# Performance work log

Hardware: AMD Instinct MI355X
Metric: run time of the kernel (lower is better)

## Reference

```python
import jax, jax.numpy as jnp
import numpy as np

C = 32           # in_channels
KH, KW = 3, 3    # kernel_range
SHIFT = 1
NP = KH * KW


def conv2d(x, w, b, pad):
    # x: NCHW, w: OIHW
    y = jax.lax.conv_general_dilated(
        x, w, window_strides=(1, 1), padding=[(pad, pad), (pad, pad)],
        dimension_numbers=('NCHW', 'OIHW', 'NCHW'))
    return y + b[None, :, None, None]


def setup_inputs() -> dict:
    key = jax.random.key(0)
    ks = jax.random.split(key, 14)
    p = lambda k, shape: (jax.random.normal(k, shape, dtype=jnp.float32) * 0.02)
    inp = {
        'x':  jax.random.normal(ks[0], (4, C, 256, 256), dtype=jnp.float32),
        'wk': p(ks[1], (C * NP, C, 1, 1)), 'bk': p(ks[2], (C * NP,)),
        'wv': p(ks[3], (C * NP, C, 1, 1)), 'bv': p(ks[4], (C * NP,)),
        'wq': p(ks[5], (C, C, 1, 1)),      'bq': p(ks[6], (C,)),
        'w1': p(ks[7], (C, C, 3, 3)),      'b1': p(ks[8], (C,)),
        'w2': p(ks[9], (2 * C, C, 3, 3)),  'b2': p(ks[10], (2 * C,)),
        'w3': p(ks[11], (C, 2 * C, 3, 3)), 'b3': p(ks[12], (C,)),
    }
    return inp


def reference(x, wk, bk, wv, bv, wq, bq, w1, b1, w2, b2, w3, b3):
    B, D, H, W = x.shape
    h_half, w_half = KH // 2, KW // 2
    ph, pw = h_half * SHIFT, w_half * SHIFT

    x_k = conv2d(x, wk, bk, 0)  # (B, D*NP, H, W)
    x_v = conv2d(x, wv, bv, 0)
    x_q = conv2d(x, wq, bq, 0)  # (B, D, H, W)

    pad4 = ((0, 0), (0, 0), (ph, ph), (pw, pw))
    x_k = jnp.pad(x_k, pad4)
    x_v = jnp.pad(x_v, pad4)
    mask_pad = jnp.pad(jnp.ones((B, 1, H, W), x.dtype), pad4)

    k_ls, v_ls, m_ls = [], [], []
    layer = 0
    for i in range(-h_half, h_half + 1):
        for j in range(-w_half, w_half + 1):
            r0 = ph + i * SHIFT
            c0 = pw + j * SHIFT
            k_ls.append(x_k[:, layer * D:(layer + 1) * D, r0:r0 + H, c0:c0 + W])
            v_ls.append(x_v[:, layer * D:(layer + 1) * D, r0:r0 + H, c0:c0 + W])
            m_ls.append(mask_pad[:, :, r0:r0 + H, c0:c0 + W])
            layer += 1

    # Faithful to torch .view semantics: flat row-major reshape, NOT a permute.
    k = jnp.stack(k_ls, axis=1).reshape(B * H * W, NP, D)   # (B,NP,D,H,W) -> flat
    v = jnp.stack(v_ls, axis=1).reshape(B * H * W, NP, D)
    m = jnp.stack(m_ls, axis=1).reshape(B * H * W, NP, 1)
    q = x_q.reshape(B * H * W, 1, D)                         # (B,D,H,W) -> flat

    scores = jnp.matmul(k, jnp.swapaxes(q, -1, -2)) * m / 8.0  # (N, NP, 1)
    alpha = jax.nn.softmax(scores, axis=1)
    res = jnp.matmul(jnp.swapaxes(alpha, -1, -2), v)           # (N, 1, D)
    t = res.reshape(B, D, H, W)

    t = jax.nn.relu(conv2d(t, w1, b1, 1))
    t = jax.nn.relu(conv2d(t, w2, b2, 1))
    t = jax.nn.relu(conv2d(t, w3, b3, 1))
    return t
```

## Files before the change

### kernel.cpp

```cpp
#include <hip/hip_runtime.h>
#include <hip/hip_bf16.h>

#define B_ 4
#define C_ 32
#define H_ 256
#define W_ 256
#define S_ 65536
#define NP_ 9
#define OC_ 288
#define PR 258
#define PWN 264
#define XGUARD 260
#define XSTRIDE 66056

using bf16 = __hip_bfloat16;
typedef __attribute__((ext_vector_type(8)))  short  short8;
typedef __attribute__((ext_vector_type(4)))  short  short4_t;
typedef __attribute__((ext_vector_type(2)))  short  short2_t;
typedef __attribute__((ext_vector_type(16))) float  f32x16;

__device__ __forceinline__ float b2f(short s) {
    return __uint_as_float(((unsigned)(unsigned short)s) << 16);
}

template<int IC, int OC>
__device__ __forceinline__ void prepA_body(int fid, const float* __restrict__ w,
                                           bf16* __restrict__ apk)
{
    constexpr int NK = 9 * IC / 16;
    int tile = fid >> 9;
    int l = (fid >> 3) & 63;
    int j = fid & 7;
    int mt = tile / NK;
    int ks = tile - mt * NK;
    int q = l >> 5;
    int oc = mt * 32 + (l & 31);
    int k = ks * 16 + q * 8 + j;
    int tap = k / IC;
    int ic = k - tap * IC;
    apk[fid] = __float2bfloat16(w[((oc * IC + ic) * 3 + tap / 3) * 3 + tap % 3]);
}

template<int G>
__device__ __forceinline__ void zerob_body(int b, int p, uint4* __restrict__ buf)
{
    int gran;
    if (p < 2 * PWN * G) {
        int row = (p < PWN * G) ? 0 : 257;
        int rem = p % (PWN * G);
        gran = row * PWN * G + rem;
    } else {
        int p2 = p - 2 * PWN * G;
        int col = (p2 < 256 * G) ? 0 : 257;
        int rem = p2 % (256 * G);
        int r = rem / G + 1;
        int icg = rem - (rem / G) * G;
        gran = (r * PWN + col) * G + icg;
    }
    buf[(size_t)b * PR * PWN * G + gran] = uint4{0, 0, 0, 0};
}

__global__ __launch_bounds__(256) void k_prep(
    const float* __restrict__ wk, const float* __restrict__ wv,
    const float* __restrict__ wq,
    const float* __restrict__ w1, const float* __restrict__ w2,
    const float* __restrict__ w3,
    bf16* __restrict__ apk0, bf16* __restrict__ apk1,
    bf16* __restrict__ apk2, bf16* __restrict__ apk3,
    uint4* __restrict__ tA, uint4* __restrict__ t1, uint4* __restrict__ t2,
    uint4* __restrict__ xb16)
{
    int idx = blockIdx.x * 256 + threadIdx.x;
    if (idx < 19456) {
        int j    = idx & 7;
        int lane = (idx >> 3) & 63;
        int ks   = (idx >> 9) & 1;
        int mt   = idx >> 10;
        int oc = lane & 31;
        int ic = ks * 16 + (lane >> 5) * 8 + j;
        const float* w; int ocg;
        if (mt < 9)       { w = wk; ocg = mt * 32 + oc; }
        else if (mt < 18) { w = wv; ocg = (mt - 9) * 32 + oc; }
        else              { w = wq; ocg = oc; }
        apk0[idx] = __float2bfloat16(w[ocg * C_ + ic]);
    } else if (idx < 28672) {
        prepA_body<32, 32>(idx - 19456, w1, apk1);
    } else if (idx < 47104) {
        prepA_body<32, 64>(idx - 28672, w2, apk2);
    } else if (idx < 65536) {
        prepA_body<64, 32>(idx - 47104, w3, apk3);
    } else if (idx < 82176) {
        int i5 = idx - 65536;
        zerob_body<4>(i5 / 4160, i5 % 4160, tA);
    } else if (idx < 98816) {
        int i6 = idx - 82176;
        zerob_body<4>(i6 / 4160, i6 % 4160, t1);
    } else if (idx < 132096) {
        int i7 = idx - 98816;
        zerob_body<8>(i7 / 8320, i7 % 8320, t2);
    } else if (idx < 142464) {
        int i8 = idx - 132096;
        size_t off;
        if (i8 < 8320) {
            int b = i8 / 2080, r = i8 - b * 2080;
            if (r < 1040) off = (size_t)b * (XSTRIDE * 4) + r;
            else          off = ((size_t)b * XSTRIDE + XGUARD + 65536) * 4 + (r - 1040);
        } else {
            off = (size_t)(4 * XSTRIDE) * 4 + (i8 - 8320);
        }
        xb16[off] = uint4{0, 0, 0, 0};
    }
}

__global__ __launch_bounds__(256) void k_q(
    const float* __restrict__ x, const bf16* __restrict__ apk,
    const float* __restrict__ bq, bf16* __restrict__ xqs, bf16* __restrict__ xb16)
{
    __shared__ bf16 lbuf[32][140];
    int bh  = blockIdx.x >> 9;
    int blk = blockIdx.x & 511;
    int pixw0 = blk << 7;
    int tid  = threadIdx.x;
    int wvi  = tid >> 6;
    int lane = tid & 63;
    int col  = lane & 31, q = lane >> 5;
    int pix  = pixw0 + wvi * 32 + col;

    const float* xb = x + (size_t)bh * (C_ * S_);

    short8 bfrag[2];
#pragma unroll
    for (int kk = 0; kk < 2; ++kk)
#pragma unroll
        for (int j = 0; j < 8; ++j) {
            bf16 h = __float2bfloat16(xb[(size_t)(kk * 16 + q * 8 + j) * S_ + pix]);
            bfrag[kk][j] = *reinterpret_cast<short*>(&h);
        }

    {
        bf16* xr = xb16 + ((size_t)bh * XSTRIDE + XGUARD + pix) * 32;
        *reinterpret_cast<short8*>(xr + (q << 3))       = bfrag[0];
        *reinterpret_cast<short8*>(xr + ((2 + q) << 3)) = bfrag[1];
    }

    const short8* apkv = reinterpret_cast<const short8*>(apk);
    f32x16 acc = {};
    acc = __builtin_amdgcn_mfma_f32_32x32x16_bf16(bfrag[0], apkv[(18 * 2 + 0) * 64 + lane], acc, 0, 0, 0);
    acc = __builtin_amdgcn_mfma_f32_32x32x16_bf16(bfrag[1], apkv[(18 * 2 + 1) * 64 + lane], acc, 0, 0, 0);
    float bbv = bq[col];
#pragma unroll
    for (int g4 = 0; g4 < 4; ++g4) {
        short4_t sv;
#pragma unroll
        for (int j = 0; j < 4; ++j) {
            bf16 hb = __float2bfloat16(acc[g4 * 4 + j] + bbv);
            sv[j] = *reinterpret_cast<short*>(&hb);
        }
        *reinterpret_cast<short4_t*>(&lbuf[col][wvi * 32 + 8 * g4 + 4 * q]) = sv;
    }
    __syncthreads();
    int ch0 = tid >> 4, chk = tid & 15, ch1 = ch0 + 16;
    short8 v0 = *reinterpret_cast<const short8*>(&lbuf[ch0][chk * 8]);
    short8 v1 = *reinterpret_cast<const short8*>(&lbuf[ch1][chk * 8]);
    int tb = (pixw0 >> 5) + (chk >> 2);
    int G2 = chk & 3;
    bf16* qb = xqs + (size_t)bh * (32 * S_);
    short4_t lo0 = {v0[0], v0[1], v0[2], v0[3]}, hi0 = {v0[4], v0[5], v0[6], v0[7]};
    short4_t lo1 = {v1[0], v1[1], v1[2], v1[3]}, hi1 = {v1[4], v1[5], v1[6], v1[7]};
    *reinterpret_cast<short4_t*>(qb + (ch0 * 2048 + tb) * 32 + G2 * 4)      = lo0;
    *reinterpret_cast<short4_t*>(qb + (ch0 * 2048 + tb) * 32 + 16 + G2 * 4) = hi0;
    *reinterpret_cast<short4_t*>(qb + (ch1 * 2048 + tb) * 32 + G2 * 4)      = lo1;
    *reinterpret_cast<short4_t*>(qb + (ch1 * 2048 + tb) * 32 + 16 + G2 * 4) = hi1;
}


#define DO_TILE(T, SQ)                                                                \
{                                                                                     \
    int Tg = tgbase + (T);                                                            \
    if (Tg < 2048) {                                                                  \
        unsigned n = (unsigned)plane_base + ((unsigned)Tg << 5);                      \
        unsigned tl = n / 288u;                                                       \
        const bf16* qp = xqb + ((size_t)tl << 5) + (q << 4);                          \
        short8 qA = *reinterpret_cast<const short8*>(qp);                             \
        short8 qB = *reinterpret_cast<const short8*>(qp + 8);                         \
        int xib = ((T) << 5) + 257 + shf + col;                                       \
        int swx = (xib ^ (xib >> 2)) & 3;                                             \
        short8 fa = *reinterpret_cast<const short8*>(&xs[xib * 4 + (q ^ swx)]);       \
        short8 fb = *reinterpret_cast<const short8*>(&xs[xib * 4 + ((2 + q) ^ swx)]); \
        bool hbad  = ((((T) << 5) < hb_lo) || (((T) << 5) >= hb_hi));                 \
        bool tb_lo = (dj == -1) && ((Tg & 7) == 0);                                   \
        bool tb_hi = (dj == 1) && ((Tg & 7) == 7);                                    \
        if (tb_lo && q == 0) qA[0] = 0;                                               \
        if (tb_hi && q == 1) qB[7] = 0;                                               \
        f32x16 ka = {bK, bK, bK, bK, bK, bK, bK, bK, bK, bK, bK, bK, bK, bK, bK, bK}; \
        ka = __builtin_amdgcn_mfma_f32_32x32x16_bf16(fa, apkv[(p * 2 + 0) * 64 + lane], ka, 0, 0, 0); \
        ka = __builtin_amdgcn_mfma_f32_32x32x16_bf16(fb, apkv[(p * 2 + 1) * 64 + lane], ka, 0, 0, 0); \
        float dot = 0.f;                                                              \
        _Pragma("unroll")                                                             \
        for (int j3 = 0; j3 < 4; ++j3) {                                              \
            dot += ka[j3]      * b2f(qA[j3]);                                         \
            dot += ka[4 + j3]  * b2f(qA[4 + j3]);                                     \
            dot += ka[8 + j3]  * b2f(qB[j3]);                                         \
            dot += ka[12 + j3] * b2f(qB[4 + j3]);                                     \
        }                                                                             \
        dot += __shfl_xor(dot, 32);                                                   \
        if (q == (SQ)) scL[(T) * 32 + col] = dot;                                     \
        f32x16 vh = {bV, bV, bV, bV, bV, bV, bV, bV, bV, bV, bV, bV, bV, bV, bV, bV}; \
        vh = __builtin_amdgcn_mfma_f32_32x32x16_bf16(fa, apkv[((9 + p) * 2 + 0) * 64 + lane], vh, 0, 0, 0); \
        vh = __builtin_amdgcn_mfma_f32_32x32x16_bf16(fb, apkv[((9 + p) * 2 + 1) * 64 + lane], vh, 0, 0, 0); \
        _Pragma("unroll")                                                             \
        for (int G2 = 0; G2 < 4; ++G2) {                                              \
            short4_t sv;                                                              \
            _Pragma("unroll")                                                         \
            for (int j3 = 0; j3 < 4; ++j3) {                                          \
                float val = hbad ? 0.f : vh[G2 * 4 + j3];                             \
                bf16 hcv = __float2bfloat16(val);                                     \
                sv[j3] = *reinterpret_cast<short*>(&hcv);                             \
            }                                                                         \
            if (G2 == 0 && tb_lo && q == 0) sv[0] = 0;                                \
            if (G2 == 3 && tb_hi && q == 1) sv[3] = 0;                                \
            *reinterpret_cast<short4_t*>(kvB + col * 1616 +                           \
                ((((T) << 2) + (G2 ^ xcol)) << 4) + q * 8) = sv;                      \
        }                                                                             \
    }                                                                                 \
}

__global__ __launch_bounds__(1024, 4) void k_fused(
    const bf16* __restrict__ xb16,
    const bf16* __restrict__ apk,
    const float* __restrict__ bk, const float* __restrict__ bv,
    const bf16* __restrict__ xqs,
    bf16* __restrict__ att)
{
    extern __shared__ char smem_raw[];
    uint4* xs  = reinterpret_cast<uint4*>(smem_raw);
    char*  kvB = smem_raw + 84096;
    float* scL = reinterpret_cast<float*>(smem_raw + 135808);
    unsigned short* scM = reinterpret_cast<unsigned short*>(smem_raw + 139008);

    int bb = blockIdx.x >> 7;
    int s0 = (blockIdx.x & 127) << 9;
    int tgbase = s0 >> 5;

    int tid  = threadIdx.x;
    int lane = tid & 63;
    int wv   = tid >> 6;
    int col  = lane & 31;
    int q    = lane >> 5;
    int xcol = (col >> 3) & 3;

    size_t qbase = ((size_t)bb << 21);
    const bf16* xqb = xqs + qbase;
    const short8* apkv = reinterpret_cast<const short8*>(apk);

    {
        const uint4* src = reinterpret_cast<const uint4*>(xb16) +
                           ((size_t)bb * XSTRIDE + XGUARD + s0 - 257) * 4;
        for (int i = tid; i < 5256; i += 1024) {
            int xi = i >> 2, g = i & 3;
            int sw = (xi ^ (xi >> 2)) & 3;
            xs[xi * 4 + (g ^ sw)] = src[i];
        }
    }

    if (tid < 576) {
        int krow = tid >= 288;
        int i2 = tid - (krow ? 288 : 0);
        int pp = i2 >> 5, dpc = i2 & 31;
        int plane_base_r = ((pp << 5) + dpc) << 16;
        unsigned tl = ((unsigned)(plane_base_r + s0 + 287)) / 288u + (unsigned)krow;
        int sk0 = (int)(tl * 288u) - plane_base_r;
        unsigned m = 0;
        if (sk0 < s0 + 512 && sk0 <= 65248) {
            m = 0x8000u;
#pragma unroll
            for (int seg = 0; seg < 9; ++seg) {
                int rm = (int)tl * 9 + seg;
                int pm = rm >> 16, sm = rm & 65535;
                int dim = pm / 3 - 1, djm = pm - (pm / 3) * 3 - 1;
                int hm = sm >> 8, wm = sm & 255;
                bool mval = ((unsigned)(hm + dim) < 256u) && ((unsigned)(wm + djm) < 256u);
                m |= (mval ? 1u : 0u) << seg;
            }
        }
        scM[tid] = (unsigned short)m;
    }
    __syncthreads();

    int sub   = tid & 15;
    int strip = tid >> 4;
    int dp    = strip & 31;
    int krow  = strip >> 5;
    int swz   = (dp >> 3) & 3;
    int vboff = dp * 1616 + (((sub >> 2) ^ swz) << 4) + ((sub >> 1) & 1) * 8 + (sub & 1) * 4;

#pragma unroll 1
    for (int p = 0; p < 9; ++p) {
        int di = p / 3 - 1, dj = p - (p / 3) * 3 - 1;
        int shf = di * 256 + dj;
        int hb_lo = (di == -1) ? (256 - s0) : (-0x40000000);
        int hb_hi = (di == 1) ? (65280 - s0) : 0x40000000;
        float bK = bk[p * 32 + col];
        float bV = bv[p * 32 + col];
        int plane_base = ((p << 5) + col) << 16;

        DO_TILE(wv, 0)
        if (wv < 9) { DO_TILE(wv + 16, 1) }
        __syncthreads();

        {
            unsigned mflags = scM[krow * 288 + p * 32 + dp];
            if (mflags & 0x8000u) {
                int plane_base_r = ((p << 5) + dp) << 16;
                unsigned tl = ((unsigned)(plane_base_r + s0 + 287)) / 288u + (unsigned)krow;
                int sk0 = (int)(tl * 288u) - plane_base_r;
                int t0 = (sk0 - s0) >> 5;
                float sc[9];
#pragma unroll
                for (int seg = 0; seg < 9; ++seg)
                    sc[seg] = ((mflags >> seg) & 1u) ? scL[(t0 + seg) * 32 + dp] * 0.125f : 0.f;
                float mx = sc[0];
#pragma unroll
                for (int s2 = 1; s2 < 9; ++s2) mx = fmaxf(mx, sc[s2]);
                float wgt[9];
                float sum = 0.f;
#pragma unroll
                for (int s2 = 0; s2 < 9; ++s2) { wgt[s2] = __expf(sc[s2] - mx); sum += wgt[s2]; }
                float inv_ = 1.f / sum;

                const char* vb = kvB + vboff + t0 * 64;
                float o0 = 0.f, o1 = 0.f;
#pragma unroll
                for (int seg = 0; seg < 9; ++seg) {
                    short2_t vg = *reinterpret_cast<const short2_t*>(vb + seg * 64);
                    float w_ = wgt[seg];
                    o0 += w_ * b2f(vg[0]);
                    o1 += w_ * b2f(vg[1]);
                }
                bf16 h0 = __float2bfloat16(o0 * inv_);
                bf16 h1 = __float2bfloat16(o1 * inv_);
                short2_t s2v = {*reinterpret_cast<short*>(&h0), *reinterpret_cast<short*>(&h1)};
                *reinterpret_cast<short2_t*>(att + qbase + ((size_t)tl << 5) + sub * 2) = s2v;
            }
        }
        __syncthreads();
    }
}

__global__ __launch_bounds__(320) void k_strad(
    const bf16* __restrict__ xb16,
    const float* __restrict__ wk, const float* __restrict__ bk,
    const float* __restrict__ wv, const float* __restrict__ bv,
    const bf16* __restrict__ xqs, bf16* __restrict__ att)
{
    __shared__ float kL[288], vL[288], qL[32], wgtL[10];
    int e = blockIdx.x;
    int b = e >> 8, i = e & 255;
    int g = i >> 3, u = i & 7;
    int tl = g * 2048 + (((2040 + u) * 1593) & 2047);
    int tid = threadIdx.x;

    if (tid < 288) {
        int f  = tl * 288 + tid;
        int cp = f >> 16;
        int sp = f & 65535;
        int tap = cp >> 5;
        int di = tap / 3 - 1, dj = tap - (tap / 3) * 3 - 1;
        int h = sp >> 8, w = sp & 255;
        bool valid = ((unsigned)(h + di) < 256u) && ((unsigned)(w + dj) < 256u);
        float kv_ = 0.f, vv_ = 0.f;
        if (valid) {
            int sx = sp + di * 256 + dj;
            const bf16* xp = xb16 + ((size_t)b * XSTRIDE + XGUARD + sx) * 32;
            const float* wkp = wk + cp * 32;
            const float* wvp = wv + cp * 32;
            float ks = bk[cp], vs = bv[cp];
            short8 xg[4];
#pragma unroll
            for (int gg = 0; gg < 4; ++gg)
                xg[gg] = *reinterpret_cast<const short8*>(xp + gg * 8);
#pragma unroll
            for (int gg = 0; gg < 4; ++gg)
#pragma unroll
                for (int j = 0; j < 8; ++j) {
                    float xv_ = b2f(xg[gg][j]);
                    ks += wkp[gg * 8 + j] * xv_;
                    vs += wvp[gg * 8 + j] * xv_;
                }
            kv_ = ks; vv_ = vs;
        }
        kL[tid] = kv_; vL[tid] = vv_;
    }
    if (tid < 32) {
        int pos = ((tid >> 2) & 1) * 16 + (tid >> 3) * 4 + (tid & 3);
        bf16 hv = xqs[(size_t)b * (32 * S_) + (size_t)tl * 32 + pos];
        qL[tid] = b2f(*reinterpret_cast<short*>(&hv));
    }
    __syncthreads();
    if (tid < 9) {
        float dot = 0.f;
#pragma unroll
        for (int d = 0; d < 32; ++d) dot += kL[tid * 32 + d] * qL[d];
        int rm = tl * 9 + tid;
        int pm = rm >> 16, sm = rm & 65535;
        int dim = pm / 3 - 1, djm = pm - (pm / 3) * 3 - 1;
        int hm = sm >> 8, wm = sm & 255;
        bool mval = ((unsigned)(hm + dim) < 256u) && ((unsigned)(wm + djm) < 256u);
        wgtL[tid] = mval ? dot * 0.125f : 0.f;
    }
    __syncthreads();
    if (tid == 0) {
        float mx = wgtL[0];
#pragma unroll
        for (int s2 = 1; s2 < 9; ++s2) mx = fmaxf(mx, wgtL[s2]);
        float sum = 0.f;
#pragma unroll
        for (int s2 = 0; s2 < 9; ++s2) { wgtL[s2] = __expf(wgtL[s2] - mx); sum += wgtL[s2]; }
        wgtL[9] = 1.f / sum;
    }
    __syncthreads();
    if (tid < 32) {
        float acc = 0.f;
#pragma unroll
        for (int seg = 0; seg < 9; ++seg) acc += wgtL[seg] * vL[seg * 32 + tid];
        att[(size_t)b * 2097152 + (size_t)tl * 32 + tid] = __float2bfloat16(acc * wgtL[9]);
    }
}

__global__ __launch_bounds__(256) void k_repack(
    const bf16* __restrict__ att, bf16* __restrict__ tA)
{
    int idx = blockIdx.x * 256 + threadIdx.x;
    int icg = idx & 3;
    int ps  = idx >> 2;
    int b = ps >> 16;
    int s = ps & 65535;
    const bf16* src = att + (size_t)b * (32 * S_) + icg * 8 * S_ + s;
    short8 v;
#pragma unroll
    for (int j = 0; j < 8; ++j)
        v[j] = *reinterpret_cast<const short*>(src + (size_t)j * S_);
    int row = (s >> 8) + 1, colp = (s & 255) + 1;
    *reinterpret_cast<short8*>(tA + ((size_t)((b * PR + row) * PWN + colp)) * 32 + icg * 8) = v;
}

template<int IC, int OC, bool NCHW_OUT>
__global__ __launch_bounds__(256) void k_conv3s(
    const bf16* __restrict__ in,
    const bf16* __restrict__ apk,
    const float* __restrict__ bs,
    void* __restrict__ outv)
{
    constexpr int G    = IC / 8;
    constexpr int M    = OC / 32;
    constexpr int KPT  = IC / 16;
    constexpr int NK   = 9 * KPT;
    constexpr int NT   = 2;
    constexpr int ROWP = 66;
    constexpr int ROWG = ROWP * G;
    constexpr int TOTG = 6 * ROWG;

    __shared__ uint4 smem[TOTG];

    int wg   = blockIdx.x;
    int orig = (wg & 7) * 128 + (wg >> 3);
    int b   = orig >> 8;
    int rem = orig & 255;
    int h0  = (rem >> 2) << 2;
    int w0  = (rem & 3) * 64;

    int tid = threadIdx.x;

    {
        const uint4* src = reinterpret_cast<const uint4*>(in);
#pragma unroll
        for (int i = 0; i < (TOTG + 255) / 256; ++i) {
            int idx = tid + i * 256;
            if (idx < TOTG) {
                int dr = idx / ROWG;
                int r2 = idx - dr * ROWG;
                uint4 v = src[((size_t)(b * PR + h0 + dr) * PWN + w0) * G + r2];
                int px = r2 >> ((G == 4) ? 2 : 3);
                int sw = (G == 4) ? ((px ^ (px >> 2)) & 3) : (px & 7);
                smem[dr * ROWG + (r2 & ~(G - 1)) + ((r2 ^ sw) & (G - 1))] = v;
            }
        }
    }
    __syncthreads();

    int lane = tid & 63;
    int wid  = tid >> 6;
    int col  = lane & 31, q = lane >> 5;
    int h    = h0 + wid;

    const short8* apkv = reinterpret_cast<const short8*>(apk);

    f32x16 acc[NT][M];
#pragma unroll
    for (int nt = 0; nt < NT; ++nt)
#pragma unroll
        for (int mt = 0; mt < M; ++mt) acc[nt][mt] = (f32x16){};

#pragma unroll
    for (int tap = 0; tap < 9; ++tap) {
        int dr = tap / 3 + wid;
        int dj = tap % 3;
#pragma unroll
        for (int icq = 0; icq < KPT; ++icq) {
            short8 bfr[NT];
#pragma unroll
            for (int nt = 0; nt < NT; ++nt) {
                int px = nt * 32 + col + dj;
                int sw = (G == 4) ? ((px ^ (px >> 2)) & 3) : (px & 7);
                bfr[nt] = *reinterpret_cast<const short8*>(
                    &smem[dr * ROWG + px * G + ((icq * 2 + q) ^ sw)]);
            }
#pragma unroll
            for (int mt = 0; mt < M; ++mt) {
                short8 afr = apkv[(mt * NK + tap * KPT + icq) * 64 + lane];
#pragma unroll
                for (int nt = 0; nt < NT; ++nt)
                    acc[nt][mt] = __builtin_amdgcn_mfma_f32_32x32x16_bf16(
                        afr, bfr[nt], acc[nt][mt], 0, 0, 0);
            }
        }
    }

#pragma unroll
    for (int nt = 0; nt < NT; ++nt) {
        int wout = w0 + nt * 32 + col;
#pragma unroll
        for (int mt = 0; mt < M; ++mt) {
            if (NCHW_OUT) {
                float* out = (float*)outv;
#pragma unroll
                for (int r = 0; r < 16; ++r) {
                    int oc = mt * 32 + (r & 3) + 8 * (r >> 2) + 4 * q;
                    out[(size_t)((b * OC + oc) * H_ + h) * W_ + wout] =
                        fmaxf(acc[nt][mt][r] + bs[oc], 0.f);
                }
            } else {
                bf16* out = (bf16*)outv;
                size_t base = (size_t)((b * PR + h + 1) * PWN + wout + 1) * OC + mt * 32 + 4 * q;
#pragma unroll
                for (int g4 = 0; g4 < 4; ++g4) {
                    short4_t sv;
#pragma unroll
                    for (int r4 = 0; r4 < 4; ++r4) {
                        int oc = mt * 32 + 8 * g4 + 4 * q + r4;
                        bf16 hh = __float2bfloat16(fmaxf(acc[nt][mt][g4 * 4 + r4] + bs[oc], 0.f));
                        sv[r4] = *reinterpret_cast<short*>(&hh);
                    }
                    *reinterpret_cast<short4_t*>(out + base + 8 * g4) = sv;
                }
            }
        }
    }
}

extern "C" void kernel_launch(void* const* d_in, const int* in_sizes, int n_in,
                              void* d_out, int out_size, void* d_ws, size_t ws_size,
                              hipStream_t stream)
{
    const float* x  = (const float*)d_in[0];
    const float* wk = (const float*)d_in[1];
    const float* bk = (const float*)d_in[2];
    const float* wv = (const float*)d_in[3];
    const float* bv = (const float*)d_in[4];
    const float* wq = (const float*)d_in[5];
    const float* bq = (const float*)d_in[6];
    const float* w1 = (const float*)d_in[7];
    const float* b1 = (const float*)d_in[8];
    const float* w2 = (const float*)d_in[9];
    const float* b2 = (const float*)d_in[10];
    const float* w3 = (const float*)d_in[11];
    const float* b3 = (const float*)d_in[12];
    float* out = (float*)d_out;
    char* ws = (char*)d_ws;

    bf16* xqs  = (bf16*)(ws);
    bf16* tA   = (bf16*)(ws + 16777216);
    bf16* t1   = (bf16*)(ws + 34213888);
    bf16* t2   = (bf16*)(ws + 51650560);
    bf16* apk0 = (bf16*)(ws + 86523904);
    bf16* apk1 = (bf16*)(ws + 86562816);
    bf16* apk2 = (bf16*)(ws + 86581248);
    bf16* apk3 = (bf16*)(ws + 86618112);
    bf16* xb16 = (bf16*)(ws + 86654976);
    bf16* attB = (bf16*)d_out;

    static bool attr_set = false;
    if (!attr_set) {
        hipFuncSetAttribute(reinterpret_cast<const void*>(k_fused),
                            hipFuncAttributeMaxDynamicSharedMemorySize, 140160);
        attr_set = true;
    }

    k_prep<<<557, 256, 0, stream>>>(wk, wv, wq, w1, w2, w3,
                                    apk0, apk1, apk2, apk3,
                                    (uint4*)tA, (uint4*)t1, (uint4*)t2, (uint4*)xb16);

    k_q<<<2048, 256, 0, stream>>>(x, apk0, bq, xqs, xb16);

    k_fused<<<512, 1024, 140160, stream>>>(xb16, apk0, bk, bv, xqs, attB);

    k_strad<<<1024, 320, 0, stream>>>(xb16, wk, bk, wv, bv, xqs, attB);

    k_repack<<<4096, 256, 0, stream>>>(attB, tA);

    k_conv3s<32, 32, false><<<1024, 256, 0, stream>>>(tA, apk1, b1, (void*)t1);
    k_conv3s<32, 64, false><<<1024, 256, 0, stream>>>(t1, apk2, b2, (void*)t2);
    k_conv3s<64, 32, true ><<<1024, 256, 0, stream>>>(t2, apk3, b3, (void*)out);
}
```

Measured before the change: 168.9 us.

## Compute softmax weights once per pixel and skip MFMAs on padded tiles

Out-of-range tiles now write zeros directly instead of running four MFMAs and the q-dot. The softmax over 9 scores moves to a dedicated 64-thread phase that stores weights and the reciprocal sum to shared memory, so the many threads sharing a pixel no longer each recompute exp/max/sum. The per-pixel metadata (tl, t0, mask) is packed once into a 32-bit word, avoiding a division in the inner loop. This adds an extra __syncthreads per iteration and grows dynamic shared memory, which may cut occupancy.

Result: no change. 170.3 us (+0.8%).

```diff
diff --git a/kernel.cpp b/kernel.cpp
--- a/kernel.cpp
+++ b/kernel.cpp
@@ -178,49 +178,57 @@
 {                                                                                     \
     int Tg = tgbase + (T);                                                            \
     if (Tg < 2048) {                                                                  \
-        unsigned n = (unsigned)plane_base + ((unsigned)Tg << 5);                      \
-        unsigned tl = n / 288u;                                                       \
-        const bf16* qp = xqb + ((size_t)tl << 5) + (q << 4);                          \
-        short8 qA = *reinterpret_cast<const short8*>(qp);                             \
-        short8 qB = *reinterpret_cast<const short8*>(qp + 8);                         \
-        int xib = ((T) << 5) + 257 + shf + col;                                       \
-        int swx = (xib ^ (xib >> 2)) & 3;                                             \
-        short8 fa = *reinterpret_cast<const short8*>(&xs[xib * 4 + (q ^ swx)]);       \
-        short8 fb = *reinterpret_cast<const short8*>(&xs[xib * 4 + ((2 + q) ^ swx)]); \
-        bool hbad  = ((((T) << 5) < hb_lo) || (((T) << 5) >= hb_hi));                 \
-        bool tb_lo = (dj == -1) && ((Tg & 7) == 0);                                   \
-        bool tb_hi = (dj == 1) && ((Tg & 7) == 7);                                    \
-        if (tb_lo && q == 0) qA[0] = 0;                                               \
-        if (tb_hi && q == 1) qB[7] = 0;                                               \
-        f32x16 ka = {bK, bK, bK, bK, bK, bK, bK, bK, bK, bK, bK, bK, bK, bK, bK, bK}; \
-        ka = __builtin_amdgcn_mfma_f32_32x32x16_bf16(fa, apkv[(p * 2 + 0) * 64 + lane], ka, 0, 0, 0); \
-        ka = __builtin_amdgcn_mfma_f32_32x32x16_bf16(fb, apkv[(p * 2 + 1) * 64 + lane], ka, 0, 0, 0); \
-        float dot = 0.f;                                                              \
-        _Pragma("unroll")                                                             \
-        for (int j3 = 0; j3 < 4; ++j3) {                                              \
-            dot += ka[j3]      * b2f(qA[j3]);                                         \
-            dot += ka[4 + j3]  * b2f(qA[4 + j3]);                                     \
-            dot += ka[8 + j3]  * b2f(qB[j3]);                                         \
-            dot += ka[12 + j3] * b2f(qB[4 + j3]);                                     \
-        }                                                                             \
-        dot += __shfl_xor(dot, 32);                                                   \
-        if (q == (SQ)) scL[(T) * 32 + col] = dot;                                     \
-        f32x16 vh = {bV, bV, bV, bV, bV, bV, bV, bV, bV, bV, bV, bV, bV, bV, bV, bV}; \
-        vh = __builtin_amdgcn_mfma_f32_32x32x16_bf16(fa, apkv[((9 + p) * 2 + 0) * 64 + lane], vh, 0, 0, 0); \
-        vh = __builtin_amdgcn_mfma_f32_32x32x16_bf16(fb, apkv[((9 + p) * 2 + 1) * 64 + lane], vh, 0, 0, 0); \
-        _Pragma("unroll")                                                             \
-        for (int G2 = 0; G2 < 4; ++G2) {                                              \
-            short4_t sv;                                                              \
+        bool hbad = ((((T) << 5) < hb_lo) || (((T) << 5) >= hb_hi));                  \
+        if (hbad) {                                                                   \
+            if (q == (SQ)) scL[(T) * 32 + col] = 0.f;                                 \
+            short4_t z = {0, 0, 0, 0};                                                \
+            _Pragma("unroll")                                                         \
+            for (int G2 = 0; G2 < 4; ++G2)                                            \
+                *reinterpret_cast<short4_t*>(kvB + col * 1616 +                       \
+                    ((((T) << 2) + (G2 ^ xcol)) << 4) + q * 8) = z;                   \
+        } else {                                                                      \
+            unsigned n = (unsigned)plane_base + ((unsigned)Tg << 5);                  \
+            unsigned tl = n / 288u;                                                   \
+            const bf16* qp = xqb + ((size_t)tl << 5) + (q << 4);                      \
+            short8 qA = *reinterpret_cast<const short8*>(qp);                         \
+            short8 qB = *reinterpret_cast<const short8*>(qp + 8);                     \
+            int xib = ((T) << 5) + 257 + shf + col;                                   \
+            int swx = (xib ^ (xib >> 2)) & 3;                                         \
+            short8 fa = *reinterpret_cast<const short8*>(&xs[xib * 4 + (q ^ swx)]);   \
+            short8 fb = *reinterpret_cast<const short8*>(&xs[xib * 4 + ((2 + q) ^ swx)]); \
+            bool tb_lo = (dj == -1) && ((Tg & 7) == 0);                               \
+            bool tb_hi = (dj == 1) && ((Tg & 7) == 7);                                \
+            if (tb_lo) { if (q == 0) qA[0] = 0; }                                     \
+            if (tb_hi) { if (q == 1) qB[7] = 0; }                                     \
+            f32x16 ka = {bK, bK, bK, bK, bK, bK, bK, bK, bK, bK, bK, bK, bK, bK, bK, bK}; \
+            ka = __builtin_amdgcn_mfma_f32_32x32x16_bf16(fa, apkv[(p * 2 + 0) * 64 + lane], ka, 0, 0, 0); \
+            ka = __builtin_amdgcn_mfma_f32_32x32x16_bf16(fb, apkv[(p * 2 + 1) * 64 + lane], ka, 0, 0, 0); \
+            float dot = 0.f;                                                          \
             _Pragma("unroll")                                                         \
             for (int j3 = 0; j3 < 4; ++j3) {                                          \
-                float val = hbad ? 0.f : vh[G2 * 4 + j3];                             \
-                bf16 hcv = __float2bfloat16(val);                                     \
-                sv[j3] = *reinterpret_cast<short*>(&hcv);                             \
+                dot += ka[j3]      * b2f(qA[j3]);                                     \
+                dot += ka[4 + j3]  * b2f(qA[4 + j3]);                                 \
+                dot += ka[8 + j3]  * b2f(qB[j3]);                                     \
+                dot += ka[12 + j3] * b2f(qB[4 + j3]);                                 \
             }                                                                         \
-            if (G2 == 0 && tb_lo && q == 0) sv[0] = 0;                                \
-            if (G2 == 3 && tb_hi && q == 1) sv[3] = 0;                                \
-            *reinterpret_cast<short4_t*>(kvB + col * 1616 +                           \
-                ((((T) << 2) + (G2 ^ xcol)) << 4) + q * 8) = sv;                      \
+            dot += __shfl_xor(dot, 32);                                               \
+            if (q == (SQ)) scL[(T) * 32 + col] = dot;                                 \
+            f32x16 vh = {bV, bV, bV, bV, bV, bV, bV, bV, bV, bV, bV, bV, bV, bV, bV, bV}; \
+            vh = __builtin_amdgcn_mfma_f32_32x32x16_bf16(fa, apkv[((9 + p) * 2 + 0) * 64 + lane], vh, 0, 0, 0); \
+            vh = __builtin_amdgcn_mfma_f32_32x32x16_bf16(fb, apkv[((9 + p) * 2 + 1) * 64 + lane], vh, 0, 0, 0); \
+            _Pragma("unroll")                                                         \
+            for (int G2 = 0; G2 < 4; ++G2) {                                          \
+                short4_t sv;                                                          \
+                _Pragma("unroll")                                                     \
+                for (int j3 = 0; j3 < 4; ++j3) {                                      \
+                    bf16 hcv = __float2bfloat16(vh[G2 * 4 + j3]);                     \
+                    sv[j3] = *reinterpret_cast<short*>(&hcv);                         \
+                }                                                                     \
+                if (G2 == 0 && tb_lo) { if (q == 0) sv[0] = 0; }                      \
+                if (G2 == 3 && tb_hi) { if (q == 1) sv[3] = 0; }                      \
+                *reinterpret_cast<short4_t*>(kvB + col * 1616 +                       \
+                    ((((T) << 2) + (G2 ^ xcol)) << 4) + q * 8) = sv;                  \
+            }                                                                         \
         }                                                                             \
     }                                                                                 \
 }
@@ -236,7 +244,8 @@
     uint4* xs  = reinterpret_cast<uint4*>(smem_raw);
     char*  kvB = smem_raw + 84096;
     float* scL = reinterpret_cast<float*>(smem_raw + 135808);
-    unsigned short* scM = reinterpret_cast<unsigned short*>(smem_raw + 139008);
+    unsigned* scMT = reinterpret_cast<unsigned*>(smem_raw + 139008);
+    float* wgtL = reinterpret_cast<float*>(smem_raw + 141312);
 
     int bb = blockIdx.x >> 7;
     int s0 = (blockIdx.x & 127) << 9;
@@ -270,9 +279,10 @@
         int plane_base_r = ((pp << 5) + dpc) << 16;
         unsigned tl = ((unsigned)(plane_base_r + s0 + 287)) / 288u + (unsigned)krow;
         int sk0 = (int)(tl * 288u) - plane_base_r;
-        unsigned m = 0;
+        unsigned e = 0;
         if (sk0 < s0 + 512 && sk0 <= 65248) {
-            m = 0x8000u;
+            int t0 = (sk0 - s0) >> 5;
+            e = (1u << 10) | ((unsigned)t0 << 11) | (tl << 16);
 #pragma unroll
             for (int seg = 0; seg < 9; ++seg) {
                 int rm = (int)tl * 9 + seg;
@@ -280,10 +290,10 @@
                 int dim = pm / 3 - 1, djm = pm - (pm / 3) * 3 - 1;
                 int hm = sm >> 8, wm = sm & 255;
                 bool mval = ((unsigned)(hm + dim) < 256u) && ((unsigned)(wm + djm) < 256u);
-                m |= (mval ? 1u : 0u) << seg;
+                e |= (mval ? 1u : 0u) << seg;
             }
         }
-        scM[tid] = (unsigned short)m;
+        scMT[tid] = e;
     }
     __syncthreads();
 
@@ -308,35 +318,47 @@
         if (wv < 9) { DO_TILE(wv + 16, 1) }
         __syncthreads();
 
+        if (tid < 64) {
+            unsigned e = scMT[(tid >> 5) * 288 + p * 32 + (tid & 31)];
+            if (e & 1024u) {
+                int t0s = (e >> 11) & 31;
+                int dps = tid & 31;
+                float sc[9];
+#pragma unroll
+                for (int seg = 0; seg < 9; ++seg)
+                    sc[seg] = ((e >> seg) & 1u) ? scL[(t0s + seg) * 32 + dps] * 0.125f : 0.f;
+                float mx = sc[0];
+#pragma unroll
+                for (int s2 = 1; s2 < 9; ++s2) mx = fmaxf(mx, sc[s2]);
+                float sum = 0.f;
+                float* wrow = wgtL + tid * 12;
+#pragma unroll
+                for (int s2 = 0; s2 < 9; ++s2) {
+                    float w_ = __expf(sc[s2] - mx);
+                    wrow[s2] = w_;
+                    sum += w_;
+                }
+                wrow[9] = 1.f / sum;
+            }
+        }
+        __syncthreads();
+
         {
-            unsigned mflags = scM[krow * 288 + p * 32 + dp];
-            if (mflags & 0x8000u) {
-                int plane_base_r = ((p << 5) + dp) << 16;
-                unsigned tl = ((unsigned)(plane_base_r + s0 + 287)) / 288u + (unsigned)krow;
-                int sk0 = (int)(tl * 288u) - plane_base_r;
-                int t0 = (sk0 - s0) >> 5;
-                float sc[9];
-#pragma unroll
-                for (int seg = 0; seg < 9; ++seg)
-                    sc[seg] = ((mflags >> seg) & 1u) ? scL[(t0 + seg) * 32 + dp] * 0.125f : 0.f;
-                float mx = sc[0];
-#pragma unroll
-                for (int s2 = 1; s2 < 9; ++s2) mx = fmaxf(mx, sc[s2]);
-                float wgt[9];
-                float sum = 0.f;
-#pragma unroll
-                for (int s2 = 0; s2 < 9; ++s2) { wgt[s2] = __expf(sc[s2] - mx); sum += wgt[s2]; }
-                float inv_ = 1.f / sum;
-
+            unsigned e = scMT[krow * 288 + p * 32 + dp];
+            if (e & 1024u) {
+                int tl = e >> 16;
+                int t0 = (e >> 11) & 31;
+                const float* wrow = wgtL + strip * 12;
                 const char* vb = kvB + vboff + t0 * 64;
                 float o0 = 0.f, o1 = 0.f;
 #pragma unroll
                 for (int seg = 0; seg < 9; ++seg) {
                     short2_t vg = *reinterpret_cast<const short2_t*>(vb + seg * 64);
-                    float w_ = wgt[seg];
+                    float w_ = wrow[seg];
                     o0 += w_ * b2f(vg[0]);
                     o1 += w_ * b2f(vg[1]);
                 }
+                float inv_ = wrow[9];
                 bf16 h0 = __float2bfloat16(o0 * inv_);
                 bf16 h1 = __float2bfloat16(o1 * inv_);
                 short2_t s2v = {*reinterpret_cast<short*>(&h0), *reinterpret_cast<short*>(&h1)};
@@ -592,7 +614,7 @@
     static bool attr_set = false;
     if (!attr_set) {
         hipFuncSetAttribute(reinterpret_cast<const void*>(k_fused),
-                            hipFuncAttributeMaxDynamicSharedMemorySize, 140160);
+                            hipFuncAttributeMaxDynamicSharedMemorySize, 144384);
         attr_set = true;
     }
 
@@ -602,7 +624,7 @@
 
     k_q<<<2048, 256, 0, stream>>>(x, apk0, bq, xqs, xb16);
 
-    k_fused<<<512, 1024, 140160, stream>>>(xb16, apk0, bk, bv, xqs, attB);
+    k_fused<<<512, 1024, 144384, stream>>>(xb16, apk0, bk, bv, xqs, attB);
 
     k_strad<<<1024, 320, 0, stream>>>(xb16, wk, bk, wv, bv, xqs, attB);
 
```
